# Optimization experiments

Hardware: AMD Instinct MI355X
Metric: run time of the kernel (lower is better)

The kernel has to match this reference:

```python
import jax, jax.numpy as jnp
import numpy as np

DIM, EXP = 512, 16
INTERNAL = DIM * EXP  # 8192
BATCH, SEQ = 2, 2048


def setup_inputs() -> dict:
    key = jax.random.key(0)
    ks = jax.random.split(key, 8)
    s = 0.02
    return {
        "x": jax.random.normal(ks[0], (BATCH, SEQ, DIM), jnp.float32),
        "W_dt_w": jax.random.normal(ks[1], (INTERNAL, DIM), jnp.float32) * s,
        "W_dt_b": jnp.zeros((INTERNAL,), jnp.float32),
        "W_B_w": jax.random.normal(ks[2], (INTERNAL, DIM), jnp.float32) * s,
        "W_B_b": jnp.zeros((INTERNAL,), jnp.float32),
        "W_C_w": jax.random.normal(ks[3], (INTERNAL, DIM), jnp.float32) * s,
        "W_C_b": jnp.zeros((INTERNAL,), jnp.float32),
        "W_V_w": jax.random.normal(ks[4], (INTERNAL, DIM), jnp.float32) * s,
        "W_V_b": jnp.zeros((INTERNAL,), jnp.float32),
        # A_log = -rand(internal): negative for stability, as in torch init
        "A_log": -jax.random.uniform(ks[5], (INTERNAL,), jnp.float32),
        "W_out_w": jax.random.normal(ks[6], (DIM, INTERNAL), jnp.float32) * s,
        "W_out_b": jnp.zeros((DIM,), jnp.float32),
    }


def _scan_combine(c1, c2):
    # semi-separable recurrence h_t = a_t * h_{t-1} + b_t, as associative op
    a1, b1 = c1
    a2, b2 = c2
    return a2 * a1, a2 * b1 + b2


def reference(x, W_dt_w, W_dt_b, W_B_w, W_B_b, W_C_w, W_C_b,
              W_V_w, W_V_b, A_log, W_out_w, W_out_b):
    # Featurizer10: discretized SSM features. Shapes: x [b,s,d] -> [b,s,n]
    dt = jax.nn.softplus(jnp.einsum('bsd,nd->bsn', x, W_dt_w) + W_dt_b)
    A_bar = jnp.exp(dt * A_log)                                  # S: [b,s,n]
    B_bar = dt * (jnp.einsum('bsd,nd->bsn', x, W_B_w) + W_B_b)   # B: [b,s,n]
    C = jnp.einsum('bsd,nd->bsn', x, W_C_w) + W_C_b              # C: [b,s,n]
    V = jnp.einsum('bsd,nd->bsn', x, W_V_w) + W_V_b              # V: [b,s,n]
    # Token mixing: h_t = A_bar_t * h_{t-1} + B_bar_t * V_t (parallel scan)
    u = B_bar * V
    _, h = jax.lax.associative_scan(_scan_combine, (A_bar, u), axis=1)
    y = C * h                                                    # [b,s,n]
    # Output projection back to model dim
    return jnp.einsum('bsn,dn->bsd', y, W_out_w) + W_out_b
```

## Files before the change

### kernel.cpp

```cpp
#include <hip/hip_runtime.h>

#define DIMK 512
#define NCH  8192
#define MTOT 4096
#define SEQL 2048
#define KS   4

typedef __attribute__((ext_vector_type(8))) short bf16x8;
typedef __attribute__((ext_vector_type(4))) float f32x4;
typedef unsigned int uint32;

__device__ __forceinline__ unsigned short f2bf(float f) {
  unsigned int u = __float_as_uint(f);
  u += 0x7fffu + ((u >> 16) & 1u);
  return (unsigned short)(u >> 16);
}
__device__ __forceinline__ float bf2f(unsigned short v) {
  return __uint_as_float(((unsigned int)v) << 16);
}

struct CvtArgs {
  const float* src[6];
  unsigned short* dst[6];
  int cum[7];
};
__global__ __launch_bounds__(256) void cvt_all_kernel(CvtArgs a, int tot) {
  const int stride = gridDim.x * 256;
  for (int i = blockIdx.x * 256 + threadIdx.x; i < tot; i += stride) {
    int s = 0;
    while (i >= a.cum[s + 1]) ++s;
    const int j = i - a.cum[s];
    const float4* sp = reinterpret_cast<const float4*>(a.src[s]);
    float4 v0 = sp[2 * j], v1 = sp[2 * j + 1];
    union { unsigned short us[8]; uint4 v; } o;
    o.us[0] = f2bf(v0.x); o.us[1] = f2bf(v0.y); o.us[2] = f2bf(v0.z); o.us[3] = f2bf(v0.w);
    o.us[4] = f2bf(v1.x); o.us[5] = f2bf(v1.y); o.us[6] = f2bf(v1.z); o.us[7] = f2bf(v1.w);
    reinterpret_cast<uint4*>(a.dst[s])[j] = o.v;
  }
}

__device__ __forceinline__ int swz(int row, int q) { return q ^ ((row >> 2) & 3); }

#define PLDS_A 4096
#define PLDS_W 8192
#define PLDS   (PLDS_A + PLDS_W)
__global__ __launch_bounds__(256) void proj_kernel(
    const unsigned short* __restrict__ xb,
    const unsigned short* __restrict__ w4,
    const float* __restrict__ b_dt, const float* __restrict__ b_B,
    const float* __restrict__ b_C, const float* __restrict__ b_V,
    const float* __restrict__ A_log,
    uint32* __restrict__ au,
    unsigned short* __restrict__ c_out)
{
  __shared__ __align__(16) unsigned short lds[3][PLDS];
  const int tid = threadIdx.x;
  const int lane = tid & 63;
  const int wave = tid >> 6;
  const int wr = wave >> 1, wc = wave & 1;
  const int id = blockIdx.x;
  const int xcd = id & 7, j = id >> 3;
  const int n0 = ((j >> 5) * 8 + xcd) * 64;
  const int m0 = (j & 31) * 128;

  auto stage = [&](int buf, int kt) {
    const int k0 = kt * 32;
    #pragma unroll
    for (int i = 0; i < 2; ++i) {
      int c = i * 256 + tid;
      int row = c >> 2, q = c & 3;
      const unsigned short* g = xb + (size_t)(m0 + row) * DIMK + k0 + swz(row, q) * 8;
      __builtin_amdgcn_global_load_lds(
          (const __attribute__((address_space(1))) void*)g,
          (__attribute__((address_space(3))) void*)&lds[buf][c * 8], 16, 0, 0);
    }
    #pragma unroll
    for (int p = 0; p < 4; ++p) {
      int row = tid >> 2, q = tid & 3;
      const unsigned short* g = w4 + ((size_t)p * NCH + n0 + row) * DIMK + k0 + swz(row, q) * 8;
      __builtin_amdgcn_global_load_lds(
          (const __attribute__((address_space(1))) void*)g,
          (__attribute__((address_space(3))) void*)&lds[buf][PLDS_A + p * 2048 + tid * 8], 16, 0, 0);
    }
  };

  f32x4 acc[4][4][2];
  #pragma unroll
  for (int p = 0; p < 4; ++p)
    #pragma unroll
    for (int fm = 0; fm < 4; ++fm)
      #pragma unroll
      for (int fn = 0; fn < 2; ++fn)
        acc[p][fm][fn] = (f32x4){0.f, 0.f, 0.f, 0.f};

  stage(0, 0);
  stage(1, 1);
  constexpr int NKT = DIMK / 32;
  #pragma unroll 1
  for (int kt = 0; kt < NKT; ++kt) {
    const int buf = kt % 3;
    if (kt < NKT - 1) asm volatile("s_waitcnt vmcnt(6)" ::: "memory");
    else              asm volatile("s_waitcnt vmcnt(0)" ::: "memory");
    __builtin_amdgcn_s_barrier();
    if (kt + 2 < NKT) stage((kt + 2) % 3, kt + 2);

    const int arow = wr * 64 + (lane & 15);
    const int qq = lane >> 4;
    bf16x8 af[4];
    #pragma unroll
    for (int fm = 0; fm < 4; ++fm) {
      const int r = arow + fm * 16;
      af[fm] = *reinterpret_cast<const bf16x8*>(&lds[buf][r * 32 + swz(r, qq) * 8]);
    }
    #pragma unroll
    for (int p = 0; p < 4; ++p) {
      bf16x8 bfr[2];
      #pragma unroll
      for (int fn = 0; fn < 2; ++fn) {
        const int r = wc * 32 + fn * 16 + (lane & 15);
        bfr[fn] = *reinterpret_cast<const bf16x8*>(
            &lds[buf][PLDS_A + p * 2048 + r * 32 + swz(r, qq) * 8]);
      }
      __builtin_amdgcn_s_setprio(1);
      #pragma unroll
      for (int fm = 0; fm < 4; ++fm)
        #pragma unroll
        for (int fn = 0; fn < 2; ++fn)
          acc[p][fm][fn] = __builtin_amdgcn_mfma_f32_16x16x32_bf16(
              af[fm], bfr[fn], acc[p][fm][fn], 0, 0, 0);
      __builtin_amdgcn_s_setprio(0);
    }
    asm volatile("s_waitcnt lgkmcnt(0)" ::: "memory");
  }

  #pragma unroll
  for (int fn = 0; fn < 2; ++fn) {
    const int n = n0 + wc * 32 + fn * 16 + (lane & 15);
    const float vbdt = b_dt[n], vbB = b_B[n], vbC = b_C[n], vbV = b_V[n];
    const float al = A_log[n];
    #pragma unroll
    for (int fm = 0; fm < 4; ++fm) {
      const int mbase = m0 + wr * 64 + fm * 16 + (lane >> 4) * 4;
      #pragma unroll
      for (int r = 0; r < 4; ++r) {
        const size_t off = (size_t)(mbase + r) * NCH + n;
        const float zdt = acc[0][fm][fn][r] + vbdt;
        const float zB  = acc[1][fm][fn][r] + vbB;
        const float zC  = acc[2][fm][fn][r] + vbC;
        const float zV  = acc[3][fm][fn][r] + vbV;
        const float dt = (zdt > 15.f) ? zdt : __logf(1.f + __expf(zdt));
        au[off] = ((uint32)f2bf(dt * al) << 16) | (uint32)f2bf(dt * zB * zV);
        c_out[off] = f2bf(zC);
      }
    }
  }
}

#define SCH 16
#define CSTEPS 128
__global__ __launch_bounds__(1024) void scan_kernel(
    const uint32* __restrict__ au,
    unsigned short* cy)
{
  __shared__ float Ap[SCH][64], He[SCH][64], H0[SCH][64];
  const int lane = threadIdx.x & 63;
  const int w = threadIdx.x >> 6;
  const int c = blockIdx.x * 64 + lane;
  const size_t base = (size_t)blockIdx.y * SEQL * NCH + (size_t)(w * CSTEPS) * NCH + c;

  {
    const uint32* ap = au + base;
    float h = 0.f, vsum = 0.f;
    #pragma unroll 1
    for (int s = 0; s < CSTEPS; s += 8) {
      uint32 wv[8];
      #pragma unroll
      for (int i = 0; i < 8; ++i) wv[i] = ap[(size_t)(s + i) * NCH];
      #pragma unroll
      for (int i = 0; i < 8; ++i) {
        const float av = bf2f((unsigned short)(wv[i] >> 16));
        const float uv = bf2f((unsigned short)(wv[i] & 0xffff));
        vsum += av;
        h = fmaf(__expf(av), h, uv);
      }
    }
    Ap[w][lane] = __expf(vsum);
    He[w][lane] = h;
  }
  __syncthreads();
  if (w == 0) {
    float run = 0.f;
    #pragma unroll
    for (int jj = 0; jj < SCH; ++jj) {
      H0[jj][lane] = run;
      run = fmaf(Ap[jj][lane], run, He[jj][lane]);
    }
  }
  __syncthreads();
  {
    const uint32* ap = au + base;
    unsigned short* cp = cy + base;
    float h = H0[w][lane];
    #pragma unroll 1
    for (int s = 0; s < CSTEPS; s += 8) {
      uint32 wv[8];
      float cv[8];
      #pragma unroll
      for (int i = 0; i < 8; ++i) {
        wv[i] = ap[(size_t)(s + i) * NCH];
        cv[i] = bf2f(cp[(size_t)(s + i) * NCH]);
      }
      #pragma unroll
      for (int i = 0; i < 8; ++i) {
        const float av = bf2f((unsigned short)(wv[i] >> 16));
        const float uv = bf2f((unsigned short)(wv[i] & 0xffff));
        h = fmaf(__expf(av), h, uv);
        cv[i] *= h;
      }
      #pragma unroll
      for (int i = 0; i < 8; ++i) cp[(size_t)(s + i) * NCH] = f2bf(cv[i]);
    }
  }
}

#define OLDS_A 4096
#define OLDS_B 2048
#define OLDS   (OLDS_A + OLDS_B)
__global__ __launch_bounds__(256) void outproj_kernel(
    const unsigned short* __restrict__ yb,
    const unsigned short* __restrict__ wout,
    float* __restrict__ partial)
{
  __shared__ __align__(16) unsigned short lds[3][OLDS];
  const int tid = threadIdx.x;
  const int lane = tid & 63;
  const int wave = tid >> 6;
  const int wr = wave >> 1, wc = wave & 1;
  const int m0 = blockIdx.x * 128;
  const int d0 = blockIdx.y * 64;
  const int kbase = blockIdx.z * (NCH / KS);

  auto stage = [&](int buf, int kt) {
    const int k0 = kbase + kt * 32;
    #pragma unroll
    for (int i = 0; i < 2; ++i) {
      int c = i * 256 + tid;
      int row = c >> 2, q = c & 3;
      const unsigned short* g = yb + (size_t)(m0 + row) * NCH + k0 + swz(row, q) * 8;
      __builtin_amdgcn_global_load_lds(
          (const __attribute__((address_space(1))) void*)g,
          (__attribute__((address_space(3))) void*)&lds[buf][c * 8], 16, 0, 0);
    }
    {
      int row = tid >> 2, q = tid & 3;
      const unsigned short* g = wout + (size_t)(d0 + row) * NCH + k0 + swz(row, q) * 8;
      __builtin_amdgcn_global_load_lds(
          (const __attribute__((address_space(1))) void*)g,
          (__attribute__((address_space(3))) void*)&lds[buf][OLDS_A + tid * 8], 16, 0, 0);
    }
  };

  f32x4 acc[4][2];
  #pragma unroll
  for (int fm = 0; fm < 4; ++fm)
    #pragma unroll
    for (int fn = 0; fn < 2; ++fn) acc[fm][fn] = (f32x4){0.f, 0.f, 0.f, 0.f};

  stage(0, 0);
  stage(1, 1);
  constexpr int NKT = (NCH / KS) / 32;
  #pragma unroll 1
  for (int kt = 0; kt < NKT; ++kt) {
    const int buf = kt % 3;
    if (kt < NKT - 1) asm volatile("s_waitcnt vmcnt(3)" ::: "memory");
    else              asm volatile("s_waitcnt vmcnt(0)" ::: "memory");
    __builtin_amdgcn_s_barrier();
    if (kt + 2 < NKT) stage((kt + 2) % 3, kt + 2);

    const int qq = lane >> 4;
    bf16x8 af[4], bfr[2];
    #pragma unroll
    for (int fm = 0; fm < 4; ++fm) {
      const int r = wr * 64 + fm * 16 + (lane & 15);
      af[fm] = *reinterpret_cast<const bf16x8*>(&lds[buf][r * 32 + swz(r, qq) * 8]);
    }
    #pragma unroll
    for (int fn = 0; fn < 2; ++fn) {
      const int r = wc * 32 + fn * 16 + (lane & 15);
      bfr[fn] = *reinterpret_cast<const bf16x8*>(
          &lds[buf][OLDS_A + r * 32 + swz(r, qq) * 8]);
    }
    __builtin_amdgcn_s_setprio(1);
    #pragma unroll
    for (int fm = 0; fm < 4; ++fm)
      #pragma unroll
      for (int fn = 0; fn < 2; ++fn)
        acc[fm][fn] = __builtin_amdgcn_mfma_f32_16x16x32_bf16(
            af[fm], bfr[fn], acc[fm][fn], 0, 0, 0);
    __builtin_amdgcn_s_setprio(0);
    asm volatile("s_waitcnt lgkmcnt(0)" ::: "memory");
  }

  float* pout = partial + (size_t)blockIdx.z * MTOT * DIMK;
  #pragma unroll
  for (int fn = 0; fn < 2; ++fn) {
    const int d = d0 + wc * 32 + fn * 16 + (lane & 15);
    #pragma unroll
    for (int fm = 0; fm < 4; ++fm) {
      const int mbase = m0 + wr * 64 + fm * 16 + (lane >> 4) * 4;
      #pragma unroll
      for (int r = 0; r < 4; ++r)
        pout[(size_t)(mbase + r) * DIMK + d] = acc[fm][fn][r];
    }
  }
}

__global__ __launch_bounds__(256) void reduce_kernel(
    const float* __restrict__ p, const float* __restrict__ bias,
    float* __restrict__ out)
{
  const int i = blockIdx.x * 256 + threadIdx.x;
  const float4* p4 = reinterpret_cast<const float4*>(p);
  float4 s = p4[i];
  #pragma unroll
  for (int k = 1; k < KS; ++k) {
    float4 t = p4[(size_t)k * (MTOT * DIMK / 4) + i];
    s.x += t.x; s.y += t.y; s.z += t.z; s.w += t.w;
  }
  const float4 b = reinterpret_cast<const float4*>(bias)[i & 127];
  s.x += b.x; s.y += b.y; s.z += b.z; s.w += b.w;
  reinterpret_cast<float4*>(out)[i] = s;
}

extern "C" void kernel_launch(void* const* d_in, const int* in_sizes, int n_in,
                              void* d_out, int out_size, void* d_ws, size_t ws_size,
                              hipStream_t stream) {
  const float* x    = (const float*)d_in[0];
  const float* Wdt  = (const float*)d_in[1];
  const float* bdt  = (const float*)d_in[2];
  const float* WB   = (const float*)d_in[3];
  const float* bB   = (const float*)d_in[4];
  const float* WC   = (const float*)d_in[5];
  const float* bC   = (const float*)d_in[6];
  const float* WV   = (const float*)d_in[7];
  const float* bV   = (const float*)d_in[8];
  const float* Alog = (const float*)d_in[9];
  const float* Wout = (const float*)d_in[10];
  const float* bout = (const float*)d_in[11];
  float* out = (float*)d_out;

  char* ws = (char*)d_ws;
  unsigned short* woutb = (unsigned short*)(ws);
  unsigned short* xb    = (unsigned short*)(ws + 8388608);
  unsigned short* w4    = (unsigned short*)(ws + 12582912);
  char* dyn = ws + 46137344;
  uint32*         au  = (uint32*)(dyn);
  unsigned short* cy  = (unsigned short*)(dyn + (size_t)MTOT * NCH * 4);
  float* partial = (float*)au;

  CvtArgs ca;
  ca.src[0] = x;    ca.dst[0] = xb;
  ca.src[1] = Wdt;  ca.dst[1] = w4 + 0 * 4194304;
  ca.src[2] = WB;   ca.dst[2] = w4 + 1 * 4194304;
  ca.src[3] = WC;   ca.dst[3] = w4 + 2 * 4194304;
  ca.src[4] = WV;   ca.dst[4] = w4 + 3 * 4194304;
  ca.src[5] = Wout; ca.dst[5] = woutb;
  ca.cum[0] = 0;        ca.cum[1] = 262144;  ca.cum[2] = 786432;
  ca.cum[3] = 1310720;  ca.cum[4] = 1835008; ca.cum[5] = 2359296;
  ca.cum[6] = 2883584;
  cvt_all_kernel<<<2048, 256, 0, stream>>>(ca, 2883584);

  proj_kernel<<<4096, 256, 0, stream>>>(
      xb, w4, bdt, bB, bC, bV, Alog, au, cy);
  scan_kernel<<<dim3(NCH / 64, 2), 1024, 0, stream>>>(au, cy);
  outproj_kernel<<<dim3(MTOT / 128, DIMK / 64, KS), 256, 0, stream>>>(
      cy, woutb, partial);
  reduce_kernel<<<MTOT * DIMK / 4 / 256, 256, 0, stream>>>(partial, bout, out);
}
```

Measured before the change: 503.8 us.

## Switch GEMM pipelines from triple to double buffering and drop XCD block remap

Both projection GEMMs move from a three-stage LDS ring to two-stage double buffering. The next tile is issued before the wait, and a second barrier per iteration guards buffer reuse. The proj kernel also drops the XCD-aware block-index swizzle in favour of a plain 2D grid. This cuts LDS use, which may allow more blocks per CU, but it shortens the prefetch distance, adds a barrier per k-step, and may lose L2 locality that the XCD mapping provided.

```diff
diff --git a/kernel.cpp b/kernel.cpp
--- a/kernel.cpp
+++ b/kernel.cpp
@@ -53,15 +53,13 @@
     uint32* __restrict__ au,
     unsigned short* __restrict__ c_out)
 {
-  __shared__ __align__(16) unsigned short lds[3][PLDS];
+  __shared__ __align__(16) unsigned short lds[2][PLDS];
   const int tid = threadIdx.x;
   const int lane = tid & 63;
   const int wave = tid >> 6;
   const int wr = wave >> 1, wc = wave & 1;
-  const int id = blockIdx.x;
-  const int xcd = id & 7, j = id >> 3;
-  const int n0 = ((j >> 5) * 8 + xcd) * 64;
-  const int m0 = (j & 31) * 128;
+  const int n0 = blockIdx.x * 64;
+  const int m0 = blockIdx.y * 128;
 
   auto stage = [&](int buf, int kt) {
     const int k0 = kt * 32;
@@ -94,15 +92,17 @@
         acc[p][fm][fn] = (f32x4){0.f, 0.f, 0.f, 0.f};
 
   stage(0, 0);
-  stage(1, 1);
   constexpr int NKT = DIMK / 32;
   #pragma unroll 1
   for (int kt = 0; kt < NKT; ++kt) {
-    const int buf = kt % 3;
-    if (kt < NKT - 1) asm volatile("s_waitcnt vmcnt(6)" ::: "memory");
-    else              asm volatile("s_waitcnt vmcnt(0)" ::: "memory");
+    const int buf = kt & 1;
+    if (kt + 1 < NKT) {
+      stage(buf ^ 1, kt + 1);
+      asm volatile("s_waitcnt vmcnt(6)" ::: "memory");
+    } else {
+      asm volatile("s_waitcnt vmcnt(0)" ::: "memory");
+    }
     __builtin_amdgcn_s_barrier();
-    if (kt + 2 < NKT) stage((kt + 2) % 3, kt + 2);
 
     const int arow = wr * 64 + (lane & 15);
     const int qq = lane >> 4;
@@ -131,6 +131,7 @@
       __builtin_amdgcn_s_setprio(0);
     }
     asm volatile("s_waitcnt lgkmcnt(0)" ::: "memory");
+    __builtin_amdgcn_s_barrier();
   }
 
   #pragma unroll
@@ -231,7 +232,7 @@
     const unsigned short* __restrict__ wout,
     float* __restrict__ partial)
 {
-  __shared__ __align__(16) unsigned short lds[3][OLDS];
+  __shared__ __align__(16) unsigned short lds[2][OLDS];
   const int tid = threadIdx.x;
   const int lane = tid & 63;
   const int wave = tid >> 6;
@@ -267,15 +268,17 @@
     for (int fn = 0; fn < 2; ++fn) acc[fm][fn] = (f32x4){0.f, 0.f, 0.f, 0.f};
 
   stage(0, 0);
-  stage(1, 1);
   constexpr int NKT = (NCH / KS) / 32;
   #pragma unroll 1
   for (int kt = 0; kt < NKT; ++kt) {
-    const int buf = kt % 3;
-    if (kt < NKT - 1) asm volatile("s_waitcnt vmcnt(3)" ::: "memory");
-    else              asm volatile("s_waitcnt vmcnt(0)" ::: "memory");
+    const int buf = kt & 1;
+    if (kt + 1 < NKT) {
+      stage(buf ^ 1, kt + 1);
+      asm volatile("s_waitcnt vmcnt(3)" ::: "memory");
+    } else {
+      asm volatile("s_waitcnt vmcnt(0)" ::: "memory");
+    }
     __builtin_amdgcn_s_barrier();
-    if (kt + 2 < NKT) stage((kt + 2) % 3, kt + 2);
 
     const int qq = lane >> 4;
     bf16x8 af[4], bfr[2];
@@ -299,6 +302,7 @@
             af[fm], bfr[fn], acc[fm][fn], 0, 0, 0);
     __builtin_amdgcn_s_setprio(0);
     asm volatile("s_waitcnt lgkmcnt(0)" ::: "memory");
+    __builtin_amdgcn_s_barrier();
   }
 
   float* pout = partial + (size_t)blockIdx.z * MTOT * DIMK;
@@ -370,7 +374,7 @@
   ca.cum[6] = 2883584;
   cvt_all_kernel<<<2048, 256, 0, stream>>>(ca, 2883584);
 
-  proj_kernel<<<4096, 256, 0, stream>>>(
+  proj_kernel<<<dim3(NCH / 64, MTOT / 128), 256, 0, stream>>>(
       xb, w4, bdt, bB, bC, bV, Alog, au, cy);
   scan_kernel<<<dim3(NCH / 64, 2), 1024, 0, stream>>>(au, cy);
   outproj_kernel<<<dim3(MTOT / 128, DIMK / 64, KS), 256, 0, stream>>>(
```

After: 488.2 us. 3.1% less time.
